# Kernel optimization log

Measured on AMD Instinct MI355X. Metric: run time of the kernel, lower is better.

Reference implementation:

```python
import math
import jax, jax.numpy as jnp
import numpy as np

T, B, E, H = 1024, 4, 1024, 16
DH = E // H
NUM_BUCKETS = 32
MAX_DISTANCE = 128


def setup_inputs() -> dict:
    key = jax.random.key(0)
    ks = jax.random.split(key, 12)
    s = 0.02
    return {
        "query": jax.random.normal(ks[0], (T, B, E), dtype=jnp.float32),
        "q_w": jax.random.normal(ks[1], (E, E), dtype=jnp.float32) * s,
        "q_b": jax.random.normal(ks[2], (E,), dtype=jnp.float32) * s,
        "k_w": jax.random.normal(ks[3], (E, E), dtype=jnp.float32) * s,
        "k_b": jax.random.normal(ks[4], (E,), dtype=jnp.float32) * s,
        "v_w": jax.random.normal(ks[5], (E, E), dtype=jnp.float32) * s,
        "v_b": jax.random.normal(ks[6], (E,), dtype=jnp.float32) * s,
        "out_w": jax.random.normal(ks[7], (E, E), dtype=jnp.float32) * s,
        "out_b": jnp.zeros((E,), dtype=jnp.float32),
        "rel_bias": jax.random.normal(ks[8], (NUM_BUCKETS, H), dtype=jnp.float32) * s,
        "grep_w": jax.random.normal(ks[9], (8, DH), dtype=jnp.float32) * s,
        "grep_b": jax.random.normal(ks[10], (8,), dtype=jnp.float32) * s,
        "grep_a": jnp.ones((1, H, 1, 1), dtype=jnp.float32),
    }


def _relative_position_buckets(qlen, klen):
    # bidirectional T5-style bucketing
    ctx = jnp.arange(qlen, dtype=jnp.int32)[:, None]
    mem = jnp.arange(klen, dtype=jnp.int32)[None, :]
    rp = mem - ctx  # [qlen, klen]
    n = NUM_BUCKETS // 2
    buckets = (rp > 0).astype(jnp.int32) * n
    arp = jnp.abs(rp)
    max_exact = n // 2
    is_small = arp < max_exact
    # guard log(0): values at arp<max_exact are never selected from the large branch
    large = max_exact + (
        jnp.log(jnp.maximum(arp, 1).astype(jnp.float32) / max_exact)
        / math.log(MAX_DISTANCE / max_exact)
        * (n - max_exact)
    ).astype(jnp.int32)
    large = jnp.minimum(large, n - 1)
    return buckets + jnp.where(is_small, arp, large)


def reference(query, q_w, q_b, k_w, k_b, v_w, v_b, out_w, out_b, rel_bias, grep_w, grep_b, grep_a):
    tgt_len, bsz, embed_dim = query.shape
    scaling = DH ** -0.5

    # relative-position bias [H, T, T]
    buckets = _relative_position_buckets(tgt_len, tgt_len)
    pos_bias = rel_bias[buckets]                     # [T, T, H]
    pos_bias = jnp.transpose(pos_bias, (2, 0, 1))    # [H, T, T]

    # GRU-style gate computed from the *unprojected* query, per head
    qh_raw = jnp.transpose(query, (1, 0, 2)).reshape(bsz, tgt_len, H, DH)
    qh_raw = jnp.transpose(qh_raw, (0, 2, 1, 3))     # [B, H, T, DH]
    g = jnp.einsum("bhtd,ed->bhte", qh_raw, grep_w) + grep_b  # [B,H,T,8]
    g = jax.nn.sigmoid(g.reshape(bsz, H, tgt_len, 2, 4).sum(-1))  # [B,H,T,2]
    gate_a, gate_b = g[..., 0:1], g[..., 1:2]        # [B,H,T,1]
    gate_a_1 = gate_a * (gate_b * grep_a - 1.0) + 2.0
    attn_bias = gate_a_1 * pos_bias[None]            # [B, H, T, T]

    # QKV projections (self-attention: k,v from query)
    q = (query @ q_w.T + q_b) * scaling
    k = query @ k_w.T + k_b
    v = query @ v_w.T + v_b
    qh = jnp.transpose(q.reshape(tgt_len, bsz, H, DH), (1, 2, 0, 3))  # [B,H,T,DH]
    kh = jnp.transpose(k.reshape(tgt_len, bsz, H, DH), (1, 2, 0, 3))
    vh = jnp.transpose(v.reshape(tgt_len, bsz, H, DH), (1, 2, 0, 3))

    scores = jnp.einsum("bhtd,bhsd->bhts", qh, kh) + attn_bias
    probs = jax.nn.softmax(scores, axis=-1)
    ctx = jnp.einsum("bhts,bhsd->bhtd", probs, vh)   # [B,H,T,DH]
    ctx = jnp.transpose(ctx, (2, 0, 1, 3)).reshape(tgt_len, bsz, embed_dim)
    out = ctx @ out_w.T + out_b                      # [T, B, E]
    return out
```

## Files before the change

kernel.cpp:

```cpp
#include <hip/hip_runtime.h>
#include <math.h>

#define T_ 1024
#define B_ 4
#define E_ 1024
#define H_ 16
#define DH_ 64

#define LOG2E 1.44269504088896f

typedef __attribute__((ext_vector_type(8))) __bf16 bf16x8;
typedef __attribute__((ext_vector_type(4))) __bf16 bf16x4;
typedef __attribute__((ext_vector_type(4))) float f32x4;

__device__ __forceinline__ __bf16 f2bf(float x){
  union { unsigned short u; __bf16 b; } cv;
  unsigned u32 = __float_as_uint(x);
  cv.u = (unsigned short)((u32 + 0x7fffu + ((u32 >> 16) & 1u)) >> 16);
  return cv.b;
}
__device__ __forceinline__ __bf16 f2bf_fast(float x){
  union { unsigned short u; __bf16 b; } cv;
  cv.u = (unsigned short)((__float_as_uint(x) + 0x8000u) >> 16);
  return cv.b;
}

__device__ __forceinline__ void glds16(const void* g, void* l){
  __builtin_amdgcn_global_load_lds(
      (__attribute__((address_space(1))) void*)(void*)g,
      (__attribute__((address_space(3))) void*)l,
      16, 0, 0);
}

__global__ __launch_bounds__(256) void prep_kernel(
    const float* __restrict__ q_w, const float* __restrict__ k_w,
    const float* __restrict__ v_w, const float* __restrict__ out_w,
    __bf16* __restrict__ wq, __bf16* __restrict__ wk,
    __bf16* __restrict__ wv, __bf16* __restrict__ wo,
    const float* __restrict__ query, const float* __restrict__ gw,
    const float* __restrict__ gb, const float* __restrict__ ga,
    float* __restrict__ gates, __bf16* __restrict__ qbf,
    const float* __restrict__ rel_bias, float* __restrict__ tab)
{
  const int bid = blockIdx.x;
  const int tid = threadIdx.x;
  if (bid < 4096){
    const float* a; __bf16* o;
    switch (bid >> 10){
      case 0: a = q_w;  o = wq; break;
      case 1: a = k_w;  o = wk; break;
      case 2: a = v_w;  o = wv; break;
      default: a = out_w; o = wo; break;
    }
    int i = ((bid & 1023) * 256 + tid) * 4;
    float4 v = *(const float4*)(a + i);
    bf16x4 r;
    r[0] = f2bf(v.x); r[1] = f2bf(v.y); r[2] = f2bf(v.z); r[3] = f2bf(v.w);
    *(bf16x4*)(o + i) = r;
  } else if (bid < 4352){
    int t = (bid - 4096) * 4 + (tid >> 6);
    int bh = tid & 63;
    int h = bh & 15;
    const float* q = query + (size_t)t * E_ * B_ + bh * 64;
    __bf16* qo = qbf + (size_t)t * E_ * B_ + bh * 64;
    float g[8];
    #pragma unroll
    for (int e = 0; e < 8; e++) g[e] = gb[e];
    #pragma unroll
    for (int c = 0; c < 8; c++){
      float4 v0 = *(const float4*)(q + c * 8);
      float4 v1 = *(const float4*)(q + c * 8 + 4);
      bf16x8 o;
      o[0] = f2bf(v0.x); o[1] = f2bf(v0.y); o[2] = f2bf(v0.z); o[3] = f2bf(v0.w);
      o[4] = f2bf(v1.x); o[5] = f2bf(v1.y); o[6] = f2bf(v1.z); o[7] = f2bf(v1.w);
      *(bf16x8*)(qo + c * 8) = o;
      #pragma unroll
      for (int e = 0; e < 8; e++){
        const float* w = gw + e * 64 + c * 8;
        g[e] += v0.x * w[0] + v0.y * w[1] + v0.z * w[2] + v0.w * w[3]
              + v1.x * w[4] + v1.y * w[5] + v1.z * w[6] + v1.w * w[7];
      }
    }
    float a0 = (g[0] + g[1]) + (g[2] + g[3]);
    float a1 = (g[4] + g[5]) + (g[6] + g[7]);
    float sa = 1.f / (1.f + __expf(-a0));
    float sb = 1.f / (1.f + __expf(-a1));
    gates[bh * T_ + t] = (sa * (sb * ga[h] - 1.0f) + 2.0f) * LOG2E;
  } else {
    int tb = bid - 4352;
    int h = tb >> 3;
    int i = (tb & 7) * 256 + tid;
    if (i < 2047){
      int rp = i - 1023;
      int base = rp > 0 ? 16 : 0;
      int arp = rp < 0 ? -rp : rp;
      int off;
      if (arp < 8) off = arp;
      else {
        float val = (logf((float)arp * 0.125f) / 2.772588722239781f) * 8.0f;
        int lg = (int)val;
        off = 8 + (lg > 7 ? 7 : lg);
      }
      tab[h * 2047 + i] = rel_bias[(base + off) * H_ + h];
    }
  }
}

__global__ __launch_bounds__(256, 2) void gemm_qkv(
    const __bf16* __restrict__ A,
    const __bf16* __restrict__ W0, const __bf16* __restrict__ W1, const __bf16* __restrict__ W2,
    const float* __restrict__ b0, const float* __restrict__ b1, const float* __restrict__ b2,
    __bf16* out0, __bf16* out1, __bf16* out2)
{
  __shared__ __bf16 As[128 * 64];
  __shared__ __bf16 Bs[3][64 * 64];
  const int tid = threadIdx.x;
  const int lane = tid & 63, wid = tid >> 6;
  const int l15 = lane & 15, quad = lane >> 4;
  const int dd = blockIdx.x;
  const int j = dd >> 3;
  const int m0 = ((dd & 7) * 4 + (j & 3)) * 128;
  const int nt = j >> 2;
  const int n0 = nt * 64;

  f32x4 acc[3][2][4];
  #pragma unroll
  for (int z = 0; z < 3; z++)
    #pragma unroll
    for (int i = 0; i < 2; i++)
      #pragma unroll
      for (int jj = 0; jj < 4; jj++){
        acc[z][i][jj][0] = 0.f; acc[z][i][jj][1] = 0.f;
        acc[z][i][jj][2] = 0.f; acc[z][i][jj][3] = 0.f;
      }

  const int grow = lane >> 3;
  const int gcol = (((lane & 7) ^ grow) * 8);
  const int sw = (l15 & 7);

  for (int k0 = 0; k0 < E_; k0 += 64){
    __syncthreads();
    #pragma unroll
    for (int r = 0; r < 4; r++){
      int rb = wid * 32 + r * 8;
      glds16(A + (size_t)(m0 + rb + grow) * E_ + k0 + gcol, &As[rb * 64]);
    }
    #pragma unroll
    for (int r = 0; r < 2; r++){
      int rb = wid * 16 + r * 8;
      glds16(W0 + (size_t)(n0 + rb + grow) * E_ + k0 + gcol, &Bs[0][rb * 64]);
      glds16(W1 + (size_t)(n0 + rb + grow) * E_ + k0 + gcol, &Bs[1][rb * 64]);
      glds16(W2 + (size_t)(n0 + rb + grow) * E_ + k0 + gcol, &Bs[2][rb * 64]);
    }
    __syncthreads();
    #pragma unroll
    for (int kq = 0; kq < 2; kq++){
      const int ce = ((kq * 4 + quad) ^ sw) * 8;
      bf16x8 am[2];
      #pragma unroll
      for (int i = 0; i < 2; i++) am[i] = *(const bf16x8*)&As[(wid * 32 + i * 16 + l15) * 64 + ce];
      #pragma unroll
      for (int z = 0; z < 3; z++){
        bf16x8 bn[4];
        #pragma unroll
        for (int jj = 0; jj < 4; jj++) bn[jj] = *(const bf16x8*)&Bs[z][(jj * 16 + l15) * 64 + ce];
        #pragma unroll
        for (int i = 0; i < 2; i++)
          #pragma unroll
          for (int jj = 0; jj < 4; jj++)
            acc[z][i][jj] = __builtin_amdgcn_mfma_f32_16x16x32_bf16(am[i], bn[jj], acc[z][i][jj], 0, 0, 0);
      }
    }
  }

  #pragma unroll
  for (int z = 0; z < 2; z++){
    __bf16* outp = z ? out1 : out0;
    const float* bias = z ? b1 : b0;
    const float scale = z ? 1.0f : 0.125f * LOG2E;
    #pragma unroll
    for (int i = 0; i < 2; i++){
      const int row0 = m0 + wid * 32 + i * 16 + quad * 4;
      #pragma unroll
      for (int jj = 0; jj < 4; jj++){
        const int col = n0 + jj * 16 + l15;
        const float bc = bias[col];
        const int d2 = col & 63;
        #pragma unroll
        for (int r = 0; r < 4; r++){
          float v = (acc[z][i][jj][r] + bc) * scale;
          int row = row0 + r;
          int t = row >> 2, bb = row & 3;
          outp[(size_t)((bb * H_ + nt) * T_ + t) * DH_ + d2] = f2bf(v);
        }
      }
    }
  }

  __syncthreads();
  __bf16 (*vbuf)[4][32] = (__bf16 (*)[4][32])&As[0];
  #pragma unroll
  for (int i = 0; i < 2; i++){
    const int t_local = wid * 8 + i * 4 + quad;
    #pragma unroll
    for (int jj = 0; jj < 4; jj++){
      const int nl = jj * 16 + l15;
      const float bc = b2[n0 + nl];
      #pragma unroll
      for (int r = 0; r < 4; r++)
        vbuf[nl][r][t_local] = f2bf(acc[2][i][jj][r] + bc);
    }
  }
  __syncthreads();
  {
    const int nl = tid >> 2;
    const int bb = tid & 3;
    __bf16* dst = out2 + (size_t)((bb * H_ + nt) * DH_ + nl) * T_ + (m0 >> 2);
    const __bf16* src = &vbuf[nl][bb][0];
    #pragma unroll
    for (int c = 0; c < 4; c++)
      *(bf16x8*)(dst + c * 8) = *(const bf16x8*)(src + c * 8);
  }
}

__global__ __launch_bounds__(256) void gemm_out(
    const __bf16* __restrict__ A, const __bf16* __restrict__ W,
    const float* __restrict__ bias, float* __restrict__ out)
{
  __shared__ __bf16 As[64 * 64];
  __shared__ __bf16 Bs[128 * 64];
  const int tid = threadIdx.x;
  const int lane = tid & 63, wid = tid >> 6;
  const int l15 = lane & 15, quad = lane >> 4;
  const int wm = wid >> 1, wn = wid & 1;
  const int dd = blockIdx.x;
  const int j = dd >> 3;
  const int m0 = ((dd & 7) * 8 + (j & 7)) * 64;
  const int n0 = (j >> 3) * 128;

  f32x4 acc[2][4];
  #pragma unroll
  for (int i = 0; i < 2; i++)
    #pragma unroll
    for (int jj = 0; jj < 4; jj++){
      acc[i][jj][0] = 0.f; acc[i][jj][1] = 0.f; acc[i][jj][2] = 0.f; acc[i][jj][3] = 0.f;
    }

  const int grow = lane >> 3;
  const int gcol = (((lane & 7) ^ grow) * 8);
  const int sw = (l15 & 7);

  for (int k0 = 0; k0 < E_; k0 += 64){
    __syncthreads();
    #pragma unroll
    for (int r = 0; r < 2; r++){
      int rbA = wid * 16 + r * 8;
      glds16(A + (size_t)(m0 + rbA + grow) * E_ + k0 + gcol, &As[rbA * 64]);
    }
    #pragma unroll
    for (int r = 0; r < 4; r++){
      int rbB = wid * 32 + r * 8;
      glds16(W + (size_t)(n0 + rbB + grow) * E_ + k0 + gcol, &Bs[rbB * 64]);
    }
    __syncthreads();
    #pragma unroll
    for (int kq = 0; kq < 2; kq++){
      const int ce = ((kq * 4 + quad) ^ sw) * 8;
      bf16x8 am[2], bn[4];
      #pragma unroll
      for (int i = 0; i < 2; i++) am[i] = *(const bf16x8*)&As[(wm * 32 + i * 16 + l15) * 64 + ce];
      #pragma unroll
      for (int jj = 0; jj < 4; jj++) bn[jj] = *(const bf16x8*)&Bs[(wn * 64 + jj * 16 + l15) * 64 + ce];
      #pragma unroll
      for (int i = 0; i < 2; i++)
        #pragma unroll
        for (int jj = 0; jj < 4; jj++)
          acc[i][jj] = __builtin_amdgcn_mfma_f32_16x16x32_bf16(am[i], bn[jj], acc[i][jj], 0, 0, 0);
    }
  }

  #pragma unroll
  for (int i = 0; i < 2; i++){
    const int row0 = m0 + wm * 32 + i * 16 + quad * 4;
    #pragma unroll
    for (int jj = 0; jj < 4; jj++){
      const int col = n0 + wn * 64 + jj * 16 + l15;
      const float bc = bias[col];
      #pragma unroll
      for (int r = 0; r < 4; r++)
        out[(size_t)(row0 + r) * E_ + col] = acc[i][jj][r] + bc;
    }
  }
}

__global__ __launch_bounds__(128) void attn_kernel(
    const __bf16* __restrict__ qg, const __bf16* __restrict__ kg, const __bf16* __restrict__ vgT,
    const float* __restrict__ gates, const float* __restrict__ tab,
    __bf16* __restrict__ ctx)
{
  const int LDP = 72;
  __shared__ __bf16 Ks[64 * 64];
  __shared__ __bf16 Vt[64 * 64];
  __shared__ __bf16 Pt[2][2][16 * LDP];
  __shared__ float tabh[2048];

  const int tid = threadIdx.x;
  const int lane = tid & 63, wid = tid >> 6;
  const int l15 = lane & 15, quad = lane >> 4;
  const int dgrid = blockIdx.x;
  const int j = dgrid >> 3;
  const int bh = (dgrid & 7) + 8 * (j & 7);
  const int tq = j >> 3;
  const int b = bh >> 4, h = bh & 15;
  const __bf16* qb = qg + (size_t)bh * T_ * DH_;
  const __bf16* kb = kg + (size_t)bh * T_ * DH_;
  const __bf16* vb = vgT + (size_t)bh * DH_ * T_;

  for (int i = tid; i < 2047; i += 128) tabh[i] = tab[h * 2047 + i];

  const int t0w = tq * 64 + wid * 32;
  bf16x8 bq[2][2];
  float g[2];
  int ibase[2];
  #pragma unroll
  for (int tg = 0; tg < 2; tg++){
    int t_lane = t0w + tg * 16 + l15;
    bq[tg][0] = *(const bf16x8*)(qb + (size_t)t_lane * DH_ + quad * 8);
    bq[tg][1] = *(const bf16x8*)(qb + (size_t)t_lane * DH_ + 32 + quad * 8);
    g[tg] = gates[bh * T_ + t_lane];
    ibase[tg] = 1023 - t_lane;
  }

  const int grow = lane >> 3;
  const int gcol = (((lane & 7) ^ grow) * 8);
  const int swf = (l15 & 7);

  float l_run[2] = {0.f, 0.f};
  f32x4 O[2][4];
  #pragma unroll
  for (int tg = 0; tg < 2; tg++)
    #pragma unroll
    for (int mt = 0; mt < 4; mt++){ O[tg][mt][0]=0.f; O[tg][mt][1]=0.f; O[tg][mt][2]=0.f; O[tg][mt][3]=0.f; }

  for (int s0 = 0; s0 < T_; s0 += 64){
    __syncthreads();
    #pragma unroll
    for (int r = 0; r < 4; r++){
      int rb = wid * 32 + r * 8;
      glds16(kb + (size_t)(s0 + rb + grow) * DH_ + gcol, &Ks[rb * 64]);
      glds16(vb + (size_t)(rb + grow) * T_ + s0 + gcol, &Vt[rb * 64]);
    }
    __syncthreads();

    f32x4 S[2][4];
    #pragma unroll
    for (int nt = 0; nt < 4; nt++){
      const int rowb = (nt * 16 + l15) * 64;
      bf16x8 ak0 = *(const bf16x8*)&Ks[rowb + ((quad ^ swf) * 8)];
      bf16x8 ak1 = *(const bf16x8*)&Ks[rowb + (((4 + quad) ^ swf) * 8)];
      #pragma unroll
      for (int tg = 0; tg < 2; tg++){
        f32x4 a; a[0]=0.f; a[1]=0.f; a[2]=0.f; a[3]=0.f;
        a = __builtin_amdgcn_mfma_f32_16x16x32_bf16(ak0, bq[tg][0], a, 0, 0, 0);
        a = __builtin_amdgcn_mfma_f32_16x16x32_bf16(ak1, bq[tg][1], a, 0, 0, 0);
        S[tg][nt] = a;
      }
    }

    const int drel = s0 - t0w;
    if (drel >= 160 || drel <= -192){
      const float sv = (drel > 0) ? tabh[1151] : tabh[895];
      #pragma unroll
      for (int tg = 0; tg < 2; tg++){
        const float cb = g[tg] * sv;
        #pragma unroll
        for (int nt = 0; nt < 4; nt++)
          #pragma unroll
          for (int r = 0; r < 4; r++)
            S[tg][nt][r] = __builtin_amdgcn_exp2f(S[tg][nt][r] + cb);
      }
    } else {
      #pragma unroll
      for (int tg = 0; tg < 2; tg++){
        const int ib = ibase[tg] + s0;
        #pragma unroll
        for (int nt = 0; nt < 4; nt++)
          #pragma unroll
          for (int r = 0; r < 4; r++)
            S[tg][nt][r] = __builtin_amdgcn_exp2f(S[tg][nt][r] + g[tg] * tabh[ib + nt * 16 + quad * 4 + r]);
      }
    }

    #pragma unroll
    for (int tg = 0; tg < 2; tg++){
      __bf16* pw = &Pt[wid][tg][0];
      #pragma unroll
      for (int nt = 0; nt < 4; nt++){
        bf16x4 p;
        p[0] = f2bf_fast(S[tg][nt][0]); p[1] = f2bf_fast(S[tg][nt][1]);
        p[2] = f2bf_fast(S[tg][nt][2]); p[3] = f2bf_fast(S[tg][nt][3]);
        *(bf16x4*)&pw[l15 * LDP + nt * 16 + quad * 4] = p;
      }
      float rs = 0.f;
      #pragma unroll
      for (int nt = 0; nt < 4; nt++) rs += (S[tg][nt][0] + S[tg][nt][1]) + (S[tg][nt][2] + S[tg][nt][3]);
      rs += __shfl_xor(rs, 16, 64);
      rs += __shfl_xor(rs, 32, 64);
      l_run[tg] += rs;
    }

    #pragma unroll
    for (int ks = 0; ks < 2; ks++){
      bf16x8 bp[2];
      #pragma unroll
      for (int tg = 0; tg < 2; tg++)
        bp[tg] = *(const bf16x8*)&Pt[wid][tg][l15 * LDP + ks * 32 + quad * 8];
      #pragma unroll
      for (int mt = 0; mt < 4; mt++){
        const int rowb = (mt * 16 + l15) * 64;
        bf16x8 av = *(const bf16x8*)&Vt[rowb + (((ks * 4 + quad) ^ swf) * 8)];
        #pragma unroll
        for (int tg = 0; tg < 2; tg++)
          O[tg][mt] = __builtin_amdgcn_mfma_f32_16x16x32_bf16(av, bp[tg], O[tg][mt], 0, 0, 0);
      }
    }
  }

  #pragma unroll
  for (int tg = 0; tg < 2; tg++){
    const int t_lane = t0w + tg * 16 + l15;
    const float inv = 1.f / l_run[tg];
    #pragma unroll
    for (int mt = 0; mt < 4; mt++){
      bf16x4 o;
      o[0] = f2bf(O[tg][mt][0] * inv); o[1] = f2bf(O[tg][mt][1] * inv);
      o[2] = f2bf(O[tg][mt][2] * inv); o[3] = f2bf(O[tg][mt][3] * inv);
      *(bf16x4*)&ctx[(size_t)(t_lane * B_ + b) * E_ + h * DH_ + mt * 16 + quad * 4] = o;
    }
  }
}

extern "C" void kernel_launch(void* const* d_in, const int* in_sizes, int n_in,
                              void* d_out, int out_size, void* d_ws, size_t ws_size,
                              hipStream_t stream)
{
  (void)in_sizes; (void)n_in; (void)out_size; (void)ws_size;
  const float* query    = (const float*)d_in[0];
  const float* q_w      = (const float*)d_in[1];
  const float* q_b      = (const float*)d_in[2];
  const float* k_w      = (const float*)d_in[3];
  const float* k_b      = (const float*)d_in[4];
  const float* v_w      = (const float*)d_in[5];
  const float* v_b      = (const float*)d_in[6];
  const float* out_w    = (const float*)d_in[7];
  const float* out_b    = (const float*)d_in[8];
  const float* rel_bias = (const float*)d_in[9];
  const float* grep_w   = (const float*)d_in[10];
  const float* grep_b   = (const float*)d_in[11];
  const float* grep_a   = (const float*)d_in[12];

  char* ws = (char*)d_ws;
  size_t off = 0;
  __bf16* qbf = (__bf16*)(ws + off); off += (size_t)4096 * 1024 * 2;
  __bf16* wq  = (__bf16*)(ws + off); off += (size_t)1024 * 1024 * 2;
  __bf16* wk  = (__bf16*)(ws + off); off += (size_t)1024 * 1024 * 2;
  __bf16* wv  = (__bf16*)(ws + off); off += (size_t)1024 * 1024 * 2;
  __bf16* wo  = (__bf16*)(ws + off); off += (size_t)1024 * 1024 * 2;
  __bf16* qh  = (__bf16*)(ws + off); off += (size_t)4096 * 1024 * 2;
  __bf16* kh  = (__bf16*)(ws + off); off += (size_t)4096 * 1024 * 2;
  __bf16* vhT = (__bf16*)(ws + off); off += (size_t)4096 * 1024 * 2;
  __bf16* ctx = (__bf16*)(ws + off); off += (size_t)4096 * 1024 * 2;
  float* gates = (float*)(ws + off); off += (size_t)65536 * 4;
  float* tab   = (float*)(ws + off); off += (size_t)16 * 2047 * 4;

  prep_kernel<<<4480, 256, 0, stream>>>(q_w, k_w, v_w, out_w, wq, wk, wv, wo,
                                        query, grep_w, grep_b, grep_a, gates, qbf,
                                        rel_bias, tab);
  gemm_qkv<<<512, 256, 0, stream>>>(qbf, wq, wk, wv, q_b, k_b, v_b, qh, kh, vhT);
  attn_kernel<<<1024, 128, 0, stream>>>(qh, kh, vhT, gates, tab, ctx);
  gemm_out<<<512, 256, 0, stream>>>(ctx, wo, out_b, (float*)d_out);
}
```

Measured before the change: 198.9 us.

## Use single-wave attention blocks with double-buffered K/V and no barriers

The attention kernel now runs one 64-lane wave per block, covering 64 query rows, in place of two waves covering 32 rows each. K/V tiles are double-buffered in LDS, and the next tile is prefetched asynchronously while the current one is computed, which removes the __syncthreads barriers. The bias table kept in shared memory shrinks to a 512-entry window, and the saturated-bias threshold changes. The cost is more registers per wave and fewer waves per block, so latency hiding depends on occupancy across blocks.

```diff
diff --git a/kernel.cpp b/kernel.cpp
--- a/kernel.cpp
+++ b/kernel.cpp
@@ -293,19 +293,17 @@
   }
 }
 
-__global__ __launch_bounds__(128) void attn_kernel(
+__global__ __launch_bounds__(64) void attn_kernel(
     const __bf16* __restrict__ qg, const __bf16* __restrict__ kg, const __bf16* __restrict__ vgT,
     const float* __restrict__ gates, const float* __restrict__ tab,
     __bf16* __restrict__ ctx)
 {
-  const int LDP = 72;
-  __shared__ __bf16 Ks[64 * 64];
-  __shared__ __bf16 Vt[64 * 64];
-  __shared__ __bf16 Pt[2][2][16 * LDP];
-  __shared__ float tabh[2048];
-
-  const int tid = threadIdx.x;
-  const int lane = tid & 63, wid = tid >> 6;
+  __shared__ __bf16 Ks[2][64 * 64];
+  __shared__ __bf16 Vt[2][64 * 64];
+  __shared__ __bf16 Pt[2][16 * 72];
+  __shared__ float tabh[512];
+
+  const int lane = threadIdx.x;
   const int l15 = lane & 15, quad = lane >> 4;
   const int dgrid = blockIdx.x;
   const int j = dgrid >> 3;
@@ -316,118 +314,118 @@
   const __bf16* kb = kg + (size_t)bh * T_ * DH_;
   const __bf16* vb = vgT + (size_t)bh * DH_ * T_;
 
-  for (int i = tid; i < 2047; i += 128) tabh[i] = tab[h * 2047 + i];
-
-  const int t0w = tq * 64 + wid * 32;
-  bf16x8 bq[2][2];
-  float g[2];
-  int ibase[2];
-  #pragma unroll
-  for (int tg = 0; tg < 2; tg++){
+  #pragma unroll
+  for (int i = 0; i < 8; i++) tabh[i * 64 + lane] = tab[h * 2047 + 768 + i * 64 + lane];
+
+  const int t0w = tq * 64;
+  bf16x8 bq[4][2];
+  float g[4];
+  #pragma unroll
+  for (int tg = 0; tg < 4; tg++){
     int t_lane = t0w + tg * 16 + l15;
     bq[tg][0] = *(const bf16x8*)(qb + (size_t)t_lane * DH_ + quad * 8);
     bq[tg][1] = *(const bf16x8*)(qb + (size_t)t_lane * DH_ + 32 + quad * 8);
     g[tg] = gates[bh * T_ + t_lane];
-    ibase[tg] = 1023 - t_lane;
   }
 
   const int grow = lane >> 3;
   const int gcol = (((lane & 7) ^ grow) * 8);
   const int swf = (l15 & 7);
 
-  float l_run[2] = {0.f, 0.f};
-  f32x4 O[2][4];
-  #pragma unroll
-  for (int tg = 0; tg < 2; tg++)
+  float l_run[4] = {0.f, 0.f, 0.f, 0.f};
+  f32x4 O[4][4];
+  #pragma unroll
+  for (int tg = 0; tg < 4; tg++)
     #pragma unroll
     for (int mt = 0; mt < 4; mt++){ O[tg][mt][0]=0.f; O[tg][mt][1]=0.f; O[tg][mt][2]=0.f; O[tg][mt][3]=0.f; }
 
+  #pragma unroll
+  for (int r = 0; r < 8; r++){
+    glds16(kb + (size_t)(r * 8 + grow) * DH_ + gcol, &Ks[0][r * 8 * 64]);
+    glds16(vb + (size_t)(r * 8 + grow) * T_ + gcol, &Vt[0][r * 8 * 64]);
+  }
+
   for (int s0 = 0; s0 < T_; s0 += 64){
-    __syncthreads();
-    #pragma unroll
-    for (int r = 0; r < 4; r++){
-      int rb = wid * 32 + r * 8;
-      glds16(kb + (size_t)(s0 + rb + grow) * DH_ + gcol, &Ks[rb * 64]);
-      glds16(vb + (size_t)(rb + grow) * T_ + s0 + gcol, &Vt[rb * 64]);
-    }
-    __syncthreads();
-
-    f32x4 S[2][4];
+    const int cur = (s0 >> 6) & 1;
+    asm volatile("s_waitcnt vmcnt(0)" ::: "memory");
+
+    bf16x8 ak[4][2], av[4][2];
     #pragma unroll
     for (int nt = 0; nt < 4; nt++){
       const int rowb = (nt * 16 + l15) * 64;
-      bf16x8 ak0 = *(const bf16x8*)&Ks[rowb + ((quad ^ swf) * 8)];
-      bf16x8 ak1 = *(const bf16x8*)&Ks[rowb + (((4 + quad) ^ swf) * 8)];
-      #pragma unroll
-      for (int tg = 0; tg < 2; tg++){
+      ak[nt][0] = *(const bf16x8*)&Ks[cur][rowb + ((quad ^ swf) * 8)];
+      ak[nt][1] = *(const bf16x8*)&Ks[cur][rowb + (((4 + quad) ^ swf) * 8)];
+      av[nt][0] = *(const bf16x8*)&Vt[cur][rowb + ((quad ^ swf) * 8)];
+      av[nt][1] = *(const bf16x8*)&Vt[cur][rowb + (((4 + quad) ^ swf) * 8)];
+    }
+
+    if (s0 + 64 < T_){
+      const int nxt = cur ^ 1;
+      const int sn = s0 + 64;
+      #pragma unroll
+      for (int r = 0; r < 8; r++){
+        glds16(kb + (size_t)(sn + r * 8 + grow) * DH_ + gcol, &Ks[nxt][r * 8 * 64]);
+        glds16(vb + (size_t)(r * 8 + grow) * T_ + sn + gcol, &Vt[nxt][r * 8 * 64]);
+      }
+    }
+
+    const int drel = s0 - t0w;
+    const bool sat = (drel >= 192) || (drel <= -192);
+    const float svc = (drel > 0) ? tabh[383] : tabh[127];
+
+    #pragma unroll
+    for (int tg = 0; tg < 4; tg++){
+      f32x4 S[4];
+      #pragma unroll
+      for (int nt = 0; nt < 4; nt++){
         f32x4 a; a[0]=0.f; a[1]=0.f; a[2]=0.f; a[3]=0.f;
-        a = __builtin_amdgcn_mfma_f32_16x16x32_bf16(ak0, bq[tg][0], a, 0, 0, 0);
-        a = __builtin_amdgcn_mfma_f32_16x16x32_bf16(ak1, bq[tg][1], a, 0, 0, 0);
-        S[tg][nt] = a;
-      }
-    }
-
-    const int drel = s0 - t0w;
-    if (drel >= 160 || drel <= -192){
-      const float sv = (drel > 0) ? tabh[1151] : tabh[895];
-      #pragma unroll
-      for (int tg = 0; tg < 2; tg++){
-        const float cb = g[tg] * sv;
+        a = __builtin_amdgcn_mfma_f32_16x16x32_bf16(ak[nt][0], bq[tg][0], a, 0, 0, 0);
+        a = __builtin_amdgcn_mfma_f32_16x16x32_bf16(ak[nt][1], bq[tg][1], a, 0, 0, 0);
+        S[nt] = a;
+      }
+      if (sat){
+        const float cb = g[tg] * svc;
         #pragma unroll
         for (int nt = 0; nt < 4; nt++)
           #pragma unroll
           for (int r = 0; r < 4; r++)
-            S[tg][nt][r] = __builtin_amdgcn_exp2f(S[tg][nt][r] + cb);
-      }
-    } else {
-      #pragma unroll
-      for (int tg = 0; tg < 2; tg++){
-        const int ib = ibase[tg] + s0;
+            S[nt][r] = __builtin_amdgcn_exp2f(S[nt][r] + cb);
+      } else {
+        const int ib = drel + 255 - tg * 16 - l15;
         #pragma unroll
         for (int nt = 0; nt < 4; nt++)
           #pragma unroll
           for (int r = 0; r < 4; r++)
-            S[tg][nt][r] = __builtin_amdgcn_exp2f(S[tg][nt][r] + g[tg] * tabh[ib + nt * 16 + quad * 4 + r]);
-      }
-    }
-
-    #pragma unroll
-    for (int tg = 0; tg < 2; tg++){
-      __bf16* pw = &Pt[wid][tg][0];
+            S[nt][r] = __builtin_amdgcn_exp2f(S[nt][r] + g[tg] * tabh[ib + nt * 16 + quad * 4 + r]);
+      }
+
+      __bf16* pw = &Pt[tg & 1][0];
       #pragma unroll
       for (int nt = 0; nt < 4; nt++){
         bf16x4 p;
-        p[0] = f2bf_fast(S[tg][nt][0]); p[1] = f2bf_fast(S[tg][nt][1]);
-        p[2] = f2bf_fast(S[tg][nt][2]); p[3] = f2bf_fast(S[tg][nt][3]);
-        *(bf16x4*)&pw[l15 * LDP + nt * 16 + quad * 4] = p;
+        p[0] = f2bf_fast(S[nt][0]); p[1] = f2bf_fast(S[nt][1]);
+        p[2] = f2bf_fast(S[nt][2]); p[3] = f2bf_fast(S[nt][3]);
+        *(bf16x4*)&pw[l15 * 72 + nt * 16 + quad * 4] = p;
       }
       float rs = 0.f;
       #pragma unroll
-      for (int nt = 0; nt < 4; nt++) rs += (S[tg][nt][0] + S[tg][nt][1]) + (S[tg][nt][2] + S[tg][nt][3]);
+      for (int nt = 0; nt < 4; nt++) rs += (S[nt][0] + S[nt][1]) + (S[nt][2] + S[nt][3]);
       rs += __shfl_xor(rs, 16, 64);
       rs += __shfl_xor(rs, 32, 64);
       l_run[tg] += rs;
-    }
-
-    #pragma unroll
-    for (int ks = 0; ks < 2; ks++){
-      bf16x8 bp[2];
-      #pragma unroll
-      for (int tg = 0; tg < 2; tg++)
-        bp[tg] = *(const bf16x8*)&Pt[wid][tg][l15 * LDP + ks * 32 + quad * 8];
-      #pragma unroll
-      for (int mt = 0; mt < 4; mt++){
-        const int rowb = (mt * 16 + l15) * 64;
-        bf16x8 av = *(const bf16x8*)&Vt[rowb + (((ks * 4 + quad) ^ swf) * 8)];
-        #pragma unroll
-        for (int tg = 0; tg < 2; tg++)
-          O[tg][mt] = __builtin_amdgcn_mfma_f32_16x16x32_bf16(av, bp[tg], O[tg][mt], 0, 0, 0);
-      }
-    }
-  }
-
-  #pragma unroll
-  for (int tg = 0; tg < 2; tg++){
+
+      #pragma unroll
+      for (int ks = 0; ks < 2; ks++){
+        bf16x8 bp = *(const bf16x8*)&pw[l15 * 72 + ks * 32 + quad * 8];
+        #pragma unroll
+        for (int mt = 0; mt < 4; mt++)
+          O[tg][mt] = __builtin_amdgcn_mfma_f32_16x16x32_bf16(av[mt][ks], bp, O[tg][mt], 0, 0, 0);
+      }
+    }
+  }
+
+  #pragma unroll
+  for (int tg = 0; tg < 4; tg++){
     const int t_lane = t0w + tg * 16 + l15;
     const float inv = 1.f / l_run[tg];
     #pragma unroll
@@ -477,6 +475,6 @@
                                         query, grep_w, grep_b, grep_a, gates, qbf,
                                         rel_bias, tab);
   gemm_qkv<<<512, 256, 0, stream>>>(qbf, wq, wk, wv, q_b, k_b, v_b, qh, kh, vhT);
-  attn_kernel<<<1024, 128, 0, stream>>>(qh, kh, vhT, gates, tab, ctx);
+  attn_kernel<<<1024, 64, 0, stream>>>(qh, kh, vhT, gates, tab, ctx);
   gemm_out<<<512, 256, 0, stream>>>(ctx, wo, out_b, (float*)d_out);
 }
```

New measurement: 204.2 us. 1.03x slower.

## Load K/V fragments directly into registers in single-wave attention blocks

Applied to the files above, without the earlier changes.

The attention kernel becomes a one-wave block of 64 threads over 32 query rows, launched on twice as many blocks. K and V tiles are no longer staged in shared memory. Each lane loads its MFMA fragments straight from global memory into registers, prefetching the next tile during compute, which removes both per-tile __syncthreads barriers. The bias table cached in shared memory is cut to the 512 entries near the diagonal. The trade-off is that K/V reuse across waves now depends on L1/L2 rather than LDS, so global traffic rises, and register pressure grows from the prefetched fragments.

```diff
diff --git a/kernel.cpp b/kernel.cpp
--- a/kernel.cpp
+++ b/kernel.cpp
@@ -293,19 +293,15 @@
   }
 }
 
-__global__ __launch_bounds__(128) void attn_kernel(
+__global__ __launch_bounds__(64, 2) void attn_kernel(
     const __bf16* __restrict__ qg, const __bf16* __restrict__ kg, const __bf16* __restrict__ vgT,
     const float* __restrict__ gates, const float* __restrict__ tab,
     __bf16* __restrict__ ctx)
 {
-  const int LDP = 72;
-  __shared__ __bf16 Ks[64 * 64];
-  __shared__ __bf16 Vt[64 * 64];
-  __shared__ __bf16 Pt[2][2][16 * LDP];
-  __shared__ float tabh[2048];
-
-  const int tid = threadIdx.x;
-  const int lane = tid & 63, wid = tid >> 6;
+  __shared__ __bf16 Pt[2][16 * 72];
+  __shared__ float tabh[512];
+
+  const int lane = threadIdx.x;
   const int l15 = lane & 15, quad = lane >> 4;
   const int dgrid = blockIdx.x;
   const int j = dgrid >> 3;
@@ -316,24 +312,22 @@
   const __bf16* kb = kg + (size_t)bh * T_ * DH_;
   const __bf16* vb = vgT + (size_t)bh * DH_ * T_;
 
-  for (int i = tid; i < 2047; i += 128) tabh[i] = tab[h * 2047 + i];
-
-  const int t0w = tq * 64 + wid * 32;
+  #pragma unroll
+  for (int i = 0; i < 8; i++) tabh[i * 64 + lane] = tab[h * 2047 + 768 + i * 64 + lane];
+
+  const int t0w = tq * 32;
   bf16x8 bq[2][2];
   float g[2];
-  int ibase[2];
   #pragma unroll
   for (int tg = 0; tg < 2; tg++){
     int t_lane = t0w + tg * 16 + l15;
     bq[tg][0] = *(const bf16x8*)(qb + (size_t)t_lane * DH_ + quad * 8);
     bq[tg][1] = *(const bf16x8*)(qb + (size_t)t_lane * DH_ + 32 + quad * 8);
     g[tg] = gates[bh * T_ + t_lane];
-    ibase[tg] = 1023 - t_lane;
-  }
-
-  const int grow = lane >> 3;
-  const int gcol = (((lane & 7) ^ grow) * 8);
-  const int swf = (l15 & 7);
+  }
+
+  const __bf16* kfrag = kb + (size_t)l15 * DH_ + quad * 8;
+  const __bf16* vfrag = vb + (size_t)l15 * T_ + quad * 8;
 
   float l_run[2] = {0.f, 0.f};
   f32x4 O[2][4];
@@ -342,64 +336,62 @@
     #pragma unroll
     for (int mt = 0; mt < 4; mt++){ O[tg][mt][0]=0.f; O[tg][mt][1]=0.f; O[tg][mt][2]=0.f; O[tg][mt][3]=0.f; }
 
+  bf16x8 ak[4][2], av[4][2];
+  #pragma unroll
+  for (int nt = 0; nt < 4; nt++){
+    ak[nt][0] = *(const bf16x8*)(kfrag + (size_t)(nt * 16) * DH_);
+    ak[nt][1] = *(const bf16x8*)(kfrag + (size_t)(nt * 16) * DH_ + 32);
+    av[nt][0] = *(const bf16x8*)(vfrag + (size_t)(nt * 16) * T_);
+    av[nt][1] = *(const bf16x8*)(vfrag + (size_t)(nt * 16) * T_ + 32);
+  }
+
   for (int s0 = 0; s0 < T_; s0 += 64){
-    __syncthreads();
-    #pragma unroll
-    for (int r = 0; r < 4; r++){
-      int rb = wid * 32 + r * 8;
-      glds16(kb + (size_t)(s0 + rb + grow) * DH_ + gcol, &Ks[rb * 64]);
-      glds16(vb + (size_t)(rb + grow) * T_ + s0 + gcol, &Vt[rb * 64]);
-    }
-    __syncthreads();
-
     f32x4 S[2][4];
     #pragma unroll
     for (int nt = 0; nt < 4; nt++){
-      const int rowb = (nt * 16 + l15) * 64;
-      bf16x8 ak0 = *(const bf16x8*)&Ks[rowb + ((quad ^ swf) * 8)];
-      bf16x8 ak1 = *(const bf16x8*)&Ks[rowb + (((4 + quad) ^ swf) * 8)];
       #pragma unroll
       for (int tg = 0; tg < 2; tg++){
         f32x4 a; a[0]=0.f; a[1]=0.f; a[2]=0.f; a[3]=0.f;
-        a = __builtin_amdgcn_mfma_f32_16x16x32_bf16(ak0, bq[tg][0], a, 0, 0, 0);
-        a = __builtin_amdgcn_mfma_f32_16x16x32_bf16(ak1, bq[tg][1], a, 0, 0, 0);
+        a = __builtin_amdgcn_mfma_f32_16x16x32_bf16(ak[nt][0], bq[tg][0], a, 0, 0, 0);
+        a = __builtin_amdgcn_mfma_f32_16x16x32_bf16(ak[nt][1], bq[tg][1], a, 0, 0, 0);
         S[tg][nt] = a;
       }
     }
 
+    const int sn = (s0 + 64) & (T_ - 1);
+    #pragma unroll
+    for (int nt = 0; nt < 4; nt++){
+      ak[nt][0] = *(const bf16x8*)(kfrag + (size_t)(sn + nt * 16) * DH_);
+      ak[nt][1] = *(const bf16x8*)(kfrag + (size_t)(sn + nt * 16) * DH_ + 32);
+    }
+
     const int drel = s0 - t0w;
-    if (drel >= 160 || drel <= -192){
-      const float sv = (drel > 0) ? tabh[1151] : tabh[895];
-      #pragma unroll
-      for (int tg = 0; tg < 2; tg++){
-        const float cb = g[tg] * sv;
+    const bool sat = (drel >= 160) || (drel <= -192);
+    const float svc = (drel > 0) ? tabh[383] : tabh[127];
+    #pragma unroll
+    for (int tg = 0; tg < 2; tg++){
+      if (sat){
+        const float cb = g[tg] * svc;
         #pragma unroll
         for (int nt = 0; nt < 4; nt++)
           #pragma unroll
           for (int r = 0; r < 4; r++)
             S[tg][nt][r] = __builtin_amdgcn_exp2f(S[tg][nt][r] + cb);
-      }
-    } else {
-      #pragma unroll
-      for (int tg = 0; tg < 2; tg++){
-        const int ib = ibase[tg] + s0;
+      } else {
+        const int ib = drel + 255 - tg * 16 - l15;
         #pragma unroll
         for (int nt = 0; nt < 4; nt++)
           #pragma unroll
           for (int r = 0; r < 4; r++)
             S[tg][nt][r] = __builtin_amdgcn_exp2f(S[tg][nt][r] + g[tg] * tabh[ib + nt * 16 + quad * 4 + r]);
       }
-    }
-
-    #pragma unroll
-    for (int tg = 0; tg < 2; tg++){
-      __bf16* pw = &Pt[wid][tg][0];
+      __bf16* pw = &Pt[tg][0];
       #pragma unroll
       for (int nt = 0; nt < 4; nt++){
         bf16x4 p;
         p[0] = f2bf_fast(S[tg][nt][0]); p[1] = f2bf_fast(S[tg][nt][1]);
         p[2] = f2bf_fast(S[tg][nt][2]); p[3] = f2bf_fast(S[tg][nt][3]);
-        *(bf16x4*)&pw[l15 * LDP + nt * 16 + quad * 4] = p;
+        *(bf16x4*)&pw[l15 * 72 + nt * 16 + quad * 4] = p;
       }
       float rs = 0.f;
       #pragma unroll
@@ -414,15 +406,18 @@
       bf16x8 bp[2];
       #pragma unroll
       for (int tg = 0; tg < 2; tg++)
-        bp[tg] = *(const bf16x8*)&Pt[wid][tg][l15 * LDP + ks * 32 + quad * 8];
-      #pragma unroll
-      for (int mt = 0; mt < 4; mt++){
-        const int rowb = (mt * 16 + l15) * 64;
-        bf16x8 av = *(const bf16x8*)&Vt[rowb + (((ks * 4 + quad) ^ swf) * 8)];
+        bp[tg] = *(const bf16x8*)&Pt[tg][l15 * 72 + ks * 32 + quad * 8];
+      #pragma unroll
+      for (int mt = 0; mt < 4; mt++)
         #pragma unroll
         for (int tg = 0; tg < 2; tg++)
-          O[tg][mt] = __builtin_amdgcn_mfma_f32_16x16x32_bf16(av, bp[tg], O[tg][mt], 0, 0, 0);
-      }
+          O[tg][mt] = __builtin_amdgcn_mfma_f32_16x16x32_bf16(av[mt][ks], bp[tg], O[tg][mt], 0, 0, 0);
+    }
+
+    #pragma unroll
+    for (int mt = 0; mt < 4; mt++){
+      av[mt][0] = *(const bf16x8*)(vfrag + (size_t)(mt * 16) * T_ + sn);
+      av[mt][1] = *(const bf16x8*)(vfrag + (size_t)(mt * 16) * T_ + sn + 32);
     }
   }
 
@@ -477,6 +472,6 @@
                                         query, grep_w, grep_b, grep_a, gates, qbf,
                                         rel_bias, tab);
   gemm_qkv<<<512, 256, 0, stream>>>(qbf, wq, wk, wv, q_b, k_b, v_b, qh, kh, vhT);
-  attn_kernel<<<1024, 128, 0, stream>>>(qh, kh, vhT, gates, tab, ctx);
+  attn_kernel<<<2048, 64, 0, stream>>>(qh, kh, vhT, gates, tab, ctx);
   gemm_out<<<512, 256, 0, stream>>>(ctx, wo, out_b, (float*)d_out);
 }
```

Measured after the change: 230.8 us. +16.0%, slower.
